# Kernel optimization log

Measured on AMD Instinct MI355X. Metric: run time of the kernel, lower is better.

Reference implementation:

```python
import jax, jax.numpy as jnp
import numpy as np


def _skew(w):
    # w: (..., 3) -> (..., 3, 3)
    wx, wy, wz = w[..., 0], w[..., 1], w[..., 2]
    z = jnp.zeros_like(wx)
    return jnp.stack([
        jnp.stack([z, -wz, wy], axis=-1),
        jnp.stack([wz, z, -wx], axis=-1),
        jnp.stack([-wy, wx, z], axis=-1),
    ], axis=-2)


def exp_se3(xi):
    # xi: (..., 6) se(3) coordinates [w, v] -> (..., 4, 4) SE(3) matrix exponential
    w = xi[..., :3]
    v = xi[..., 3:]
    th2 = jnp.sum(w * w, axis=-1)
    small = th2 < 1e-12
    th2_safe = jnp.where(small, 1.0, th2)
    th = jnp.sqrt(th2_safe)
    # Rodrigues coefficients with small-angle Taylor fallbacks
    A = jnp.where(small, 1.0 - th2 / 6.0, jnp.sin(th) / th)
    B = jnp.where(small, 0.5 - th2 / 24.0, (1.0 - jnp.cos(th)) / th2_safe)
    C = jnp.where(small, 1.0 / 6.0 - th2 / 120.0, (th - jnp.sin(th)) / (th2_safe * th))
    W = _skew(w)
    W2 = W @ W
    I3 = jnp.eye(3, dtype=xi.dtype)
    R = I3 + A[..., None, None] * W + B[..., None, None] * W2
    V = I3 + B[..., None, None] * W + C[..., None, None] * W2
    p = jnp.einsum('...ij,...j->...i', V, v)
    top = jnp.concatenate([R, p[..., None]], axis=-1)            # (..., 3, 4)
    bottom_row = jnp.array([0.0, 0.0, 0.0, 1.0], dtype=xi.dtype)
    bot = jnp.broadcast_to(bottom_row, top.shape[:-2] + (1, 4))  # (..., 1, 4)
    return jnp.concatenate([top, bot], axis=-2)


def setup_inputs() -> dict:
    key = jax.random.key(0)
    k1, k2, k3 = jax.random.split(key, 3)
    nBatch, nJoint = 262144, 24
    x = jax.random.normal(k1, (nBatch, nJoint), dtype=jnp.float32)
    # eta ~ U(-1, 1) per torch init (stdv = 1)
    eta = jax.random.uniform(k2, (nJoint, 6), dtype=jnp.float32, minval=-1.0, maxval=1.0)
    # M_se3 ~ U(-2, 2)
    M_se3 = jax.random.uniform(k3, (1, 6), dtype=jnp.float32, minval=-2.0, maxval=2.0)
    return {"x": x, "eta": eta, "M_se3": M_se3}


def reference(x, eta, M_se3):
    # x: (B, nJoint) joint angles; eta: (nJoint, 6) joint twists (useAdjoint=False);
    # M_se3: (1, 6) home pose in se(3).
    nBatch = x.shape[0]
    joint_twist = eta  # getJointTwist() with useAdjoint=False

    def step(T, inp):
        twist, ang = inp                                  # (6,), (B,)
        E = exp_se3(ang[:, None] * twist[None, :])        # (B, 4, 4)
        return T @ E, None

    T0 = jnp.broadcast_to(jnp.eye(4, dtype=x.dtype), (nBatch, 4, 4))
    T, _ = jax.lax.scan(step, T0, (joint_twist, x.T))
    return T @ exp_se3(M_se3)  # (B,4,4) @ (1,4,4) broadcasts over batch
```

## Files before the change

### kernel.cpp

```cpp
#include <hip/hip_runtime.h>

#define NJ   24
#define BLK  256
#define JREC 5
#define QMF4 (NJ * JREC)
#define NCPY (NJ * JREC + 2)
#define INV4PI 0.07957747154594767f

struct DQ { float w, x, y, z, t0, t1, t2; };

__device__ __forceinline__ DQ dq_comp(const DQ A, const DQ B) {
    const float u10 = A.y*B.t2 - A.z*B.t1;
    const float u11 = A.z*B.t0 - A.x*B.t2;
    const float u12 = A.x*B.t1 - A.y*B.t0;
    const float u20 = A.y*u12 - A.z*u11;
    const float u21 = A.z*u10 - A.x*u12;
    const float u22 = A.x*u11 - A.y*u10;
    const float tw  = 2.0f * A.w;
    DQ C;
    C.t0 = fmaf(tw, u10, fmaf(2.0f, u20, A.t0 + B.t0));
    C.t1 = fmaf(tw, u11, fmaf(2.0f, u21, A.t1 + B.t1));
    C.t2 = fmaf(tw, u12, fmaf(2.0f, u22, A.t2 + B.t2));
    C.w = A.w*B.w - A.x*B.x - A.y*B.y - A.z*B.z;
    C.x = A.w*B.x + A.x*B.w + A.y*B.z - A.z*B.y;
    C.y = A.w*B.y - A.x*B.z + A.y*B.w + A.z*B.x;
    C.z = A.w*B.z + A.x*B.y - A.y*B.x + A.z*B.w;
    return C;
}

__device__ __forceinline__ DQ dq_exp(const float4 A4, const float4 B4,
                                     const float4 C4, const float4 D4,
                                     const float a) {
    const float hrev = a * B4.w;
    const float sh   = __builtin_amdgcn_sinf(hrev);
    const float ch   = __builtin_amdgcn_cosf(hrev);
    const float s    = 2.0f * sh * ch;
    const float cB   = 2.0f * sh * sh;
    const float phi  = a * A4.w;
    const float g    = phi - s;
    DQ e;
    e.w  = ch;
    e.x  = sh * A4.x;
    e.y  = sh * A4.y;
    e.z  = sh * A4.z;
    e.t0 = fmaf(a, B4.x, fmaf(cB, C4.x, g * D4.x));
    e.t1 = fmaf(a, B4.y, fmaf(cB, C4.y, g * D4.y));
    e.t2 = fmaf(a, B4.z, fmaf(cB, C4.z, g * D4.z));
    return e;
}

__global__ __launch_bounds__(BLK, 4)
void poe_main(const float* __restrict__ x,
              const float* __restrict__ eta,
              const float* __restrict__ M,
              float* __restrict__ out,
              int nBatch)
{
    __shared__ float4 sC[NCPY];
    float* sF = (float*)sC;

    const int t = threadIdx.x;
    if (t < NJ) {
        const float w0 = eta[t*6+0], w1 = eta[t*6+1], w2 = eta[t*6+2];
        const float v0 = eta[t*6+3], v1 = eta[t*6+4], v2 = eta[t*6+5];
        const float k  = w0*w0 + w1*w1 + w2*w2;
        const bool  sm = (k < 1e-12f);
        const float invsqk = sm ? 0.0f : rsqrtf(k);
        const float sqk    = k * invsqk;
        const float invk   = invsqk * invsqk;
        const float invk15 = invk * invsqk;
        const float c10 = w1*v2 - w2*v1;
        const float c11 = w2*v0 - w0*v2;
        const float c12 = w0*v1 - w1*v0;
        const float c20 = w1*c12 - w2*c11;
        const float c21 = w2*c10 - w0*c12;
        const float c22 = w0*c11 - w1*c10;
        float* r = sF + t * JREC * 4;
        r[0]  = w0*invsqk;  r[1]  = w1*invsqk;  r[2]  = w2*invsqk;  r[3]  = sqk;
        r[4]  = v0;         r[5]  = v1;         r[6]  = v2;         r[7]  = sqk * INV4PI;
        r[8]  = c10*invk;   r[9]  = c11*invk;   r[10] = c12*invk;   r[11] = 0.0f;
        r[12] = c20*invk15; r[13] = c21*invk15; r[14] = c22*invk15; r[15] = 0.0f;
    } else if (t == NJ) {
        const float w0 = M[0], w1 = M[1], w2 = M[2];
        const float v0 = M[3], v1 = M[4], v2 = M[5];
        const float t2 = w0*w0 + w1*w1 + w2*w2;
        const bool  sm = (t2 < 1e-12f);
        const float t2s  = sm ? 1.0f : t2;
        const float invt = rsqrtf(t2s);
        const float th   = t2s * invt;
        float s, c;
        __sincosf(th, &s, &c);
        const float invt2 = invt * invt;
        const float B = sm ? 0.5f        : (1.0f - c) * invt2;
        const float C = sm ? (1.0f/6.0f) : (th - s) * invt2 * invt;
        float sh, chh;
        __sincosf(0.5f * th, &sh, &chh);
        const float axs = sm ? 0.5f : sh * invt;
        float* r = sF + QMF4 * 4;
        r[0] = sm ? 1.0f : chh;
        r[1] = axs * w0;
        r[2] = axs * w1;
        r[3] = axs * w2;
        const float c10 = w1*v2 - w2*v1, c11 = w2*v0 - w0*v2, c12 = w0*v1 - w1*v0;
        const float c20 = w1*c12 - w2*c11, c21 = w2*c10 - w0*c12, c22 = w0*c11 - w1*c10;
        r[4] = v0 + B*c10 + C*c20;
        r[5] = v1 + B*c11 + C*c21;
        r[6] = v2 + B*c12 + C*c22;
        r[7] = 0.0f;
    }

    const int gid = blockIdx.x * BLK + t;
    const int row = gid >> 2;
    const int q   = gid & 3;
    const bool active = row < nBatch;

    float2 xa = make_float2(0.f,0.f), xb = xa, xc = xa;
    if (active) {
        const float2* xp = (const float2*)(x + (size_t)row * NJ + q * 6);
        xa = xp[0]; xb = xp[1]; xc = xp[2];
    }

    __syncthreads();

    const int cbase = q * 6 * JREC;

#define REC(JJ, S) sC[cbase + (JJ)*JREC + (S)]

    const DQ e0 = dq_exp(REC(0,0), REC(0,1), REC(0,2), REC(0,3), xa.x);
    const DQ e1 = dq_exp(REC(1,0), REC(1,1), REC(1,2), REC(1,3), xa.y);
    const DQ e2 = dq_exp(REC(2,0), REC(2,1), REC(2,2), REC(2,3), xb.x);
    const DQ e3 = dq_exp(REC(3,0), REC(3,1), REC(3,2), REC(3,3), xb.y);
    const DQ e4 = dq_exp(REC(4,0), REC(4,1), REC(4,2), REC(4,3), xc.x);
    const DQ e5 = dq_exp(REC(5,0), REC(5,1), REC(5,2), REC(5,3), xc.y);
#undef REC

    const DQ c01 = dq_comp(e0, e1);
    const DQ c23 = dq_comp(e2, e3);
    const DQ c45 = dq_comp(e4, e5);
    const DQ c03 = dq_comp(c01, c23);
    DQ T = dq_comp(c03, c45);

#define COMBINE(BIT) do {                                                     \
    DQ O;                                                                     \
    O.w  = __shfl_xor(T.w,  BIT);  O.x  = __shfl_xor(T.x,  BIT);              \
    O.y  = __shfl_xor(T.y,  BIT);  O.z  = __shfl_xor(T.z,  BIT);              \
    O.t0 = __shfl_xor(T.t0, BIT);  O.t1 = __shfl_xor(T.t1, BIT);              \
    O.t2 = __shfl_xor(T.t2, BIT);                                             \
    const bool up = (q & (BIT)) != 0;          \
    DQ A, B;                                                                  \
    A.w  = up ? O.w  : T.w;   B.w  = up ? T.w  : O.w;                         \
    A.x  = up ? O.x  : T.x;   B.x  = up ? T.x  : O.x;                         \
    A.y  = up ? O.y  : T.y;   B.y  = up ? T.y  : O.y;                         \
    A.z  = up ? O.z  : T.z;   B.z  = up ? T.z  : O.z;                         \
    A.t0 = up ? O.t0 : T.t0;  B.t0 = up ? T.t0 : O.t0;                        \
    A.t1 = up ? O.t1 : T.t1;  B.t1 = up ? T.t1 : O.t1;                        \
    A.t2 = up ? O.t2 : T.t2;  B.t2 = up ? T.t2 : O.t2;                        \
    T = dq_comp(A, B);                                                        \
} while (0)

    COMBINE(1);
    COMBINE(2);
#undef COMBINE

    {
        const float4 Qm = sC[QMF4];
        const float4 Pm = sC[QMF4 + 1];
        DQ Em;
        Em.w = Qm.x; Em.x = Qm.y; Em.y = Qm.z; Em.z = Qm.w;
        Em.t0 = Pm.x; Em.t1 = Pm.y; Em.t2 = Pm.z;
        T = dq_comp(T, Em);
    }

    if (active) {
        const float xx = T.x*T.x, yy = T.y*T.y, zz = T.z*T.z;
        const float xy = T.x*T.y, xz = T.x*T.z, yz = T.y*T.z;
        const float wx = T.w*T.x, wy = T.w*T.y, wz = T.w*T.z;
        const float R00 = 1.0f - 2.0f*(yy + zz);
        const float R01 = 2.0f*(xy - wz);
        const float R02 = 2.0f*(xz + wy);
        const float R10 = 2.0f*(xy + wz);
        const float R11 = 1.0f - 2.0f*(xx + zz);
        const float R12 = 2.0f*(yz - wx);
        const float R20 = 2.0f*(xz - wy);
        const float R21 = 2.0f*(yz + wx);
        const float R22 = 1.0f - 2.0f*(xx + yy);

        float4 mine;
        if      (q == 0) mine = make_float4(R00, R01, R02, T.t0);
        else if (q == 1) mine = make_float4(R10, R11, R12, T.t1);
        else if (q == 2) mine = make_float4(R20, R21, R22, T.t2);
        else             mine = make_float4(0.0f, 0.0f, 0.0f, 1.0f);

        ((float4*)out)[(size_t)row * 4 + q] = mine;
    }
}

extern "C" void kernel_launch(void* const* d_in, const int* in_sizes, int n_in,
                              void* d_out, int out_size, void* d_ws, size_t ws_size,
                              hipStream_t stream)
{
    const float* x   = (const float*)d_in[0];
    const float* eta = (const float*)d_in[1];
    const float* M   = (const float*)d_in[2];
    float* out = (float*)d_out;

    const int nBatch   = in_sizes[0] / NJ;
    const int nThreads = nBatch * 4;
    const int grid     = (nThreads + BLK - 1) / BLK;

    poe_main<<<grid, BLK, 0, stream>>>(x, eta, M, out, nBatch);
}
```

Measured before the change: 21.24 us.

## Process four rows per thread with register-cached joint constants and prefetch

```diff
diff --git a/kernel.cpp b/kernel.cpp
--- a/kernel.cpp
+++ b/kernel.cpp
@@ -2,12 +2,16 @@
 
 #define NJ   24
 #define BLK  256
+#define W    4
 #define JREC 5
 #define QMF4 (NJ * JREC)
 #define NCPY (NJ * JREC + 2)
 #define INV4PI 0.07957747154594767f
+#define FOURPI 12.566370614359172f
 
 struct DQ { float w, x, y, z, t0, t1, t2; };
+
+struct JC { float W0,W1,W2,h, v0,v1,v2, c10,c11,c12, c20,c21,c22; };
 
 __device__ __forceinline__ DQ dq_comp(const DQ A, const DQ B) {
     const float u10 = A.y*B.t2 - A.z*B.t1;
@@ -28,24 +32,21 @@
     return C;
 }
 
-__device__ __forceinline__ DQ dq_exp(const float4 A4, const float4 B4,
-                                     const float4 C4, const float4 D4,
-                                     const float a) {
-    const float hrev = a * B4.w;
+__device__ __forceinline__ DQ dq_exp(const JC J, const float a) {
+    const float hrev = a * J.h;
     const float sh   = __builtin_amdgcn_sinf(hrev);
     const float ch   = __builtin_amdgcn_cosf(hrev);
     const float s    = 2.0f * sh * ch;
     const float cB   = 2.0f * sh * sh;
-    const float phi  = a * A4.w;
-    const float g    = phi - s;
+    const float g    = fmaf(FOURPI, hrev, -s);
     DQ e;
     e.w  = ch;
-    e.x  = sh * A4.x;
-    e.y  = sh * A4.y;
-    e.z  = sh * A4.z;
-    e.t0 = fmaf(a, B4.x, fmaf(cB, C4.x, g * D4.x));
-    e.t1 = fmaf(a, B4.y, fmaf(cB, C4.y, g * D4.y));
-    e.t2 = fmaf(a, B4.z, fmaf(cB, C4.z, g * D4.z));
+    e.x  = sh * J.W0;
+    e.y  = sh * J.W1;
+    e.z  = sh * J.W2;
+    e.t0 = fmaf(a, J.v0, fmaf(cB, J.c10, g * J.c20));
+    e.t1 = fmaf(a, J.v1, fmaf(cB, J.c11, g * J.c21));
+    e.t2 = fmaf(a, J.v2, fmaf(cB, J.c12, g * J.c22));
     return e;
 }
 
@@ -109,89 +110,105 @@
         r[7] = 0.0f;
     }
 
-    const int gid = blockIdx.x * BLK + t;
-    const int row = gid >> 2;
-    const int q   = gid & 3;
-    const bool active = row < nBatch;
-
+    const int gid    = blockIdx.x * BLK + t;
+    const int tq     = gid >> 2;
+    const int q      = gid & 3;
+    const int stride = (gridDim.x * BLK) >> 2;
+
+    __syncthreads();
+
+    JC jc[6];
+    const int cbase = q * 6 * JREC;
+    #pragma unroll
+    for (int j = 0; j < 6; ++j) {
+        const float4 A4 = sC[cbase + j*JREC + 0];
+        const float4 B4 = sC[cbase + j*JREC + 1];
+        const float4 C4 = sC[cbase + j*JREC + 2];
+        const float4 D4 = sC[cbase + j*JREC + 3];
+        jc[j].W0 = A4.x; jc[j].W1 = A4.y; jc[j].W2 = A4.z; jc[j].h = B4.w;
+        jc[j].v0 = B4.x; jc[j].v1 = B4.y; jc[j].v2 = B4.z;
+        jc[j].c10 = C4.x; jc[j].c11 = C4.y; jc[j].c12 = C4.z;
+        jc[j].c20 = D4.x; jc[j].c21 = D4.y; jc[j].c22 = D4.z;
+    }
+
+    const float4 Qm = sC[QMF4];
+    const float4 Pm = sC[QMF4 + 1];
+    DQ Em;
+    Em.w = Qm.x; Em.x = Qm.y; Em.y = Qm.z; Em.z = Qm.w;
+    Em.t0 = Pm.x; Em.t1 = Pm.y; Em.t2 = Pm.z;
+
+    int row = tq;
     float2 xa = make_float2(0.f,0.f), xb = xa, xc = xa;
-    if (active) {
+    if (row < nBatch) {
         const float2* xp = (const float2*)(x + (size_t)row * NJ + q * 6);
         xa = xp[0]; xb = xp[1]; xc = xp[2];
     }
 
-    __syncthreads();
-
-    const int cbase = q * 6 * JREC;
-
-#define REC(JJ, S) sC[cbase + (JJ)*JREC + (S)]
-
-    const DQ e0 = dq_exp(REC(0,0), REC(0,1), REC(0,2), REC(0,3), xa.x);
-    const DQ e1 = dq_exp(REC(1,0), REC(1,1), REC(1,2), REC(1,3), xa.y);
-    const DQ e2 = dq_exp(REC(2,0), REC(2,1), REC(2,2), REC(2,3), xb.x);
-    const DQ e3 = dq_exp(REC(3,0), REC(3,1), REC(3,2), REC(3,3), xb.y);
-    const DQ e4 = dq_exp(REC(4,0), REC(4,1), REC(4,2), REC(4,3), xc.x);
-    const DQ e5 = dq_exp(REC(5,0), REC(5,1), REC(5,2), REC(5,3), xc.y);
-#undef REC
-
-    const DQ c01 = dq_comp(e0, e1);
-    const DQ c23 = dq_comp(e2, e3);
-    const DQ c45 = dq_comp(e4, e5);
-    const DQ c03 = dq_comp(c01, c23);
-    DQ T = dq_comp(c03, c45);
+    #pragma unroll
+    for (int i = 0; i < W; ++i) {
+        const int nrow = row + stride;
+        float2 nxa = make_float2(0.f,0.f), nxb = nxa, nxc = nxa;
+        if (i < W-1 && nrow < nBatch) {
+            const float2* xp = (const float2*)(x + (size_t)nrow * NJ + q * 6);
+            nxa = xp[0]; nxb = xp[1]; nxc = xp[2];
+        }
+
+        DQ T = dq_exp(jc[0], xa.x);
+        T = dq_comp(T, dq_exp(jc[1], xa.y));
+        T = dq_comp(T, dq_exp(jc[2], xb.x));
+        T = dq_comp(T, dq_exp(jc[3], xb.y));
+        T = dq_comp(T, dq_exp(jc[4], xc.x));
+        T = dq_comp(T, dq_exp(jc[5], xc.y));
 
 #define COMBINE(BIT) do {                                                     \
-    DQ O;                                                                     \
-    O.w  = __shfl_xor(T.w,  BIT);  O.x  = __shfl_xor(T.x,  BIT);              \
-    O.y  = __shfl_xor(T.y,  BIT);  O.z  = __shfl_xor(T.z,  BIT);              \
-    O.t0 = __shfl_xor(T.t0, BIT);  O.t1 = __shfl_xor(T.t1, BIT);              \
-    O.t2 = __shfl_xor(T.t2, BIT);                                             \
-    const bool up = (q & (BIT)) != 0;          \
-    DQ A, B;                                                                  \
-    A.w  = up ? O.w  : T.w;   B.w  = up ? T.w  : O.w;                         \
-    A.x  = up ? O.x  : T.x;   B.x  = up ? T.x  : O.x;                         \
-    A.y  = up ? O.y  : T.y;   B.y  = up ? T.y  : O.y;                         \
-    A.z  = up ? O.z  : T.z;   B.z  = up ? T.z  : O.z;                         \
-    A.t0 = up ? O.t0 : T.t0;  B.t0 = up ? T.t0 : O.t0;                        \
-    A.t1 = up ? O.t1 : T.t1;  B.t1 = up ? T.t1 : O.t1;                        \
-    A.t2 = up ? O.t2 : T.t2;  B.t2 = up ? T.t2 : O.t2;                        \
-    T = dq_comp(A, B);                                                        \
+        DQ O;                                                                 \
+        O.w  = __shfl_xor(T.w,  BIT);  O.x  = __shfl_xor(T.x,  BIT);          \
+        O.y  = __shfl_xor(T.y,  BIT);  O.z  = __shfl_xor(T.z,  BIT);          \
+        O.t0 = __shfl_xor(T.t0, BIT);  O.t1 = __shfl_xor(T.t1, BIT);          \
+        O.t2 = __shfl_xor(T.t2, BIT);                                         \
+        const bool up = (q & (BIT)) != 0;      \
+        DQ A, B;                                                              \
+        A.w  = up ? O.w  : T.w;   B.w  = up ? T.w  : O.w;                     \
+        A.x  = up ? O.x  : T.x;   B.x  = up ? T.x  : O.x;                     \
+        A.y  = up ? O.y  : T.y;   B.y  = up ? T.y  : O.y;                     \
+        A.z  = up ? O.z  : T.z;   B.z  = up ? T.z  : O.z;                     \
+        A.t0 = up ? O.t0 : T.t0;  B.t0 = up ? T.t0 : O.t0;                    \
+        A.t1 = up ? O.t1 : T.t1;  B.t1 = up ? T.t1 : O.t1;                    \
+        A.t2 = up ? O.t2 : T.t2;  B.t2 = up ? T.t2 : O.t2;                    \
+        T = dq_comp(A, B);                                                    \
 } while (0)
 
-    COMBINE(1);
-    COMBINE(2);
+        COMBINE(1);
+        COMBINE(2);
 #undef COMBINE
 
-    {
-        const float4 Qm = sC[QMF4];
-        const float4 Pm = sC[QMF4 + 1];
-        DQ Em;
-        Em.w = Qm.x; Em.x = Qm.y; Em.y = Qm.z; Em.z = Qm.w;
-        Em.t0 = Pm.x; Em.t1 = Pm.y; Em.t2 = Pm.z;
         T = dq_comp(T, Em);
-    }
-
-    if (active) {
-        const float xx = T.x*T.x, yy = T.y*T.y, zz = T.z*T.z;
-        const float xy = T.x*T.y, xz = T.x*T.z, yz = T.y*T.z;
-        const float wx = T.w*T.x, wy = T.w*T.y, wz = T.w*T.z;
-        const float R00 = 1.0f - 2.0f*(yy + zz);
-        const float R01 = 2.0f*(xy - wz);
-        const float R02 = 2.0f*(xz + wy);
-        const float R10 = 2.0f*(xy + wz);
-        const float R11 = 1.0f - 2.0f*(xx + zz);
-        const float R12 = 2.0f*(yz - wx);
-        const float R20 = 2.0f*(xz - wy);
-        const float R21 = 2.0f*(yz + wx);
-        const float R22 = 1.0f - 2.0f*(xx + yy);
-
-        float4 mine;
-        if      (q == 0) mine = make_float4(R00, R01, R02, T.t0);
-        else if (q == 1) mine = make_float4(R10, R11, R12, T.t1);
-        else if (q == 2) mine = make_float4(R20, R21, R22, T.t2);
-        else             mine = make_float4(0.0f, 0.0f, 0.0f, 1.0f);
-
-        ((float4*)out)[(size_t)row * 4 + q] = mine;
+
+        if (row < nBatch) {
+            const float xx = T.x*T.x, yy = T.y*T.y, zz = T.z*T.z;
+            const float xy = T.x*T.y, xz = T.x*T.z, yz = T.y*T.z;
+            const float wx = T.w*T.x, wy = T.w*T.y, wz = T.w*T.z;
+            const float R00 = 1.0f - 2.0f*(yy + zz);
+            const float R01 = 2.0f*(xy - wz);
+            const float R02 = 2.0f*(xz + wy);
+            const float R10 = 2.0f*(xy + wz);
+            const float R11 = 1.0f - 2.0f*(xx + zz);
+            const float R12 = 2.0f*(yz - wx);
+            const float R20 = 2.0f*(xz - wy);
+            const float R21 = 2.0f*(yz + wx);
+            const float R22 = 1.0f - 2.0f*(xx + yy);
+
+            float4 mine;
+            if      (q == 0) mine = make_float4(R00, R01, R02, T.t0);
+            else if (q == 1) mine = make_float4(R10, R11, R12, T.t1);
+            else if (q == 2) mine = make_float4(R20, R21, R22, T.t2);
+            else             mine = make_float4(0.0f, 0.0f, 0.0f, 1.0f);
+
+            ((float4*)out)[(size_t)row * 4 + q] = mine;
+        }
+
+        row = nrow;
+        xa = nxa; xb = nxb; xc = nxc;
     }
 }
 
@@ -205,7 +222,8 @@
     float* out = (float*)d_out;
 
     const int nBatch   = in_sizes[0] / NJ;
-    const int nThreads = nBatch * 4;
+    const int nQuads   = (nBatch + W - 1) / W;
+    const int nThreads = nQuads * 4;
     const int grid     = (nThreads + BLK - 1) / BLK;
 
     poe_main<<<grid, BLK, 0, stream>>>(x, eta, M, out, nBatch);
```

Measured after the change: 24.59 us. 1.16x slower.

## Assign joint groups per wavefront, broadcast twist constants via readlane, reduce through LDS

Applied to the files above, without the earlier changes.

```diff
diff --git a/kernel.cpp b/kernel.cpp
--- a/kernel.cpp
+++ b/kernel.cpp
@@ -2,12 +2,16 @@
 
 #define NJ   24
 #define BLK  256
-#define JREC 5
-#define QMF4 (NJ * JREC)
-#define NCPY (NJ * JREC + 2)
+#define RPB  64
+#define SDS  36
 #define INV4PI 0.07957747154594767f
+#define FOURPI 12.566370614359172f
 
 struct DQ { float w, x, y, z, t0, t1, t2; };
+
+__device__ __forceinline__ float rdl(float v, int l) {
+    return __int_as_float(__builtin_amdgcn_readlane(__float_as_int(v), l));
+}
 
 __device__ __forceinline__ DQ dq_comp(const DQ A, const DQ B) {
     const float u10 = A.y*B.t2 - A.z*B.t1;
@@ -28,62 +32,99 @@
     return C;
 }
 
-__device__ __forceinline__ DQ dq_exp(const float4 A4, const float4 B4,
-                                     const float4 C4, const float4 D4,
-                                     const float a) {
-    const float hrev = a * B4.w;
+__device__ __forceinline__ DQ dq_exp(float W0, float W1, float W2, float hh,
+                                     float v0, float v1, float v2,
+                                     float c10, float c11, float c12,
+                                     float c20, float c21, float c22,
+                                     float a) {
+    const float hrev = a * hh;
     const float sh   = __builtin_amdgcn_sinf(hrev);
     const float ch   = __builtin_amdgcn_cosf(hrev);
     const float s    = 2.0f * sh * ch;
     const float cB   = 2.0f * sh * sh;
-    const float phi  = a * A4.w;
-    const float g    = phi - s;
+    const float g    = fmaf(FOURPI, hrev, -s);
     DQ e;
     e.w  = ch;
-    e.x  = sh * A4.x;
-    e.y  = sh * A4.y;
-    e.z  = sh * A4.z;
-    e.t0 = fmaf(a, B4.x, fmaf(cB, C4.x, g * D4.x));
-    e.t1 = fmaf(a, B4.y, fmaf(cB, C4.y, g * D4.y));
-    e.t2 = fmaf(a, B4.z, fmaf(cB, C4.z, g * D4.z));
+    e.x  = sh * W0;
+    e.y  = sh * W1;
+    e.z  = sh * W2;
+    e.t0 = fmaf(a, v0, fmaf(cB, c10, g * c20));
+    e.t1 = fmaf(a, v1, fmaf(cB, c11, g * c21));
+    e.t2 = fmaf(a, v2, fmaf(cB, c12, g * c22));
     return e;
 }
 
-__global__ __launch_bounds__(BLK, 4)
+__global__ __launch_bounds__(BLK, 8)
 void poe_main(const float* __restrict__ x,
               const float* __restrict__ eta,
               const float* __restrict__ M,
               float* __restrict__ out,
               int nBatch)
 {
-    __shared__ float4 sC[NCPY];
-    float* sF = (float*)sC;
+    __shared__ float sD[RPB * SDS];
 
-    const int t = threadIdx.x;
-    if (t < NJ) {
-        const float w0 = eta[t*6+0], w1 = eta[t*6+1], w2 = eta[t*6+2];
-        const float v0 = eta[t*6+3], v1 = eta[t*6+4], v2 = eta[t*6+5];
-        const float k  = w0*w0 + w1*w1 + w2*w2;
+    const int t    = threadIdx.x;
+    const int lane = t & 63;
+    const int w    = __builtin_amdgcn_readfirstlane(t >> 6);
+
+    const int row  = blockIdx.x * RPB + lane;
+    const bool active = row < nBatch;
+
+    float2 xa = make_float2(0.f,0.f), xb = xa, xc = xa;
+    if (active) {
+        const float2* xp = (const float2*)(x + (size_t)row * NJ + w * 6);
+        xa = xp[0]; xb = xp[1]; xc = xp[2];
+    }
+
+    float W0,W1,W2,hh, v0,v1,v2, c10,c11,c12, c20,c21,c22;
+    {
+        const int jj = w*6 + (lane < 6 ? lane : 0);
+        const float e0 = eta[jj*6+0], e1 = eta[jj*6+1], e2 = eta[jj*6+2];
+        const float e3 = eta[jj*6+3], e4 = eta[jj*6+4], e5 = eta[jj*6+5];
+        const float k  = e0*e0 + e1*e1 + e2*e2;
         const bool  sm = (k < 1e-12f);
         const float invsqk = sm ? 0.0f : rsqrtf(k);
         const float sqk    = k * invsqk;
         const float invk   = invsqk * invsqk;
         const float invk15 = invk * invsqk;
-        const float c10 = w1*v2 - w2*v1;
-        const float c11 = w2*v0 - w0*v2;
-        const float c12 = w0*v1 - w1*v0;
-        const float c20 = w1*c12 - w2*c11;
-        const float c21 = w2*c10 - w0*c12;
-        const float c22 = w0*c11 - w1*c10;
-        float* r = sF + t * JREC * 4;
-        r[0]  = w0*invsqk;  r[1]  = w1*invsqk;  r[2]  = w2*invsqk;  r[3]  = sqk;
-        r[4]  = v0;         r[5]  = v1;         r[6]  = v2;         r[7]  = sqk * INV4PI;
-        r[8]  = c10*invk;   r[9]  = c11*invk;   r[10] = c12*invk;   r[11] = 0.0f;
-        r[12] = c20*invk15; r[13] = c21*invk15; r[14] = c22*invk15; r[15] = 0.0f;
-    } else if (t == NJ) {
-        const float w0 = M[0], w1 = M[1], w2 = M[2];
-        const float v0 = M[3], v1 = M[4], v2 = M[5];
-        const float t2 = w0*w0 + w1*w1 + w2*w2;
+        W0 = e0*invsqk; W1 = e1*invsqk; W2 = e2*invsqk;
+        hh = sqk * INV4PI;
+        v0 = e3; v1 = e4; v2 = e5;
+        const float a0 = e1*e5 - e2*e4;
+        const float a1 = e2*e3 - e0*e5;
+        const float a2 = e0*e4 - e1*e3;
+        c10 = a0*invk;  c11 = a1*invk;  c12 = a2*invk;
+        c20 = (e1*a2 - e2*a1)*invk15;
+        c21 = (e2*a0 - e0*a2)*invk15;
+        c22 = (e0*a1 - e1*a0)*invk15;
+    }
+
+#define EXPJ(J, A_) dq_exp(rdl(W0,J), rdl(W1,J), rdl(W2,J), rdl(hh,J),       \
+                           rdl(v0,J), rdl(v1,J), rdl(v2,J),                  \
+                           rdl(c10,J), rdl(c11,J), rdl(c12,J),               \
+                           rdl(c20,J), rdl(c21,J), rdl(c22,J), (A_))
+
+    DQ T = EXPJ(0, xa.x);
+    T = dq_comp(T, EXPJ(1, xa.y));
+    T = dq_comp(T, EXPJ(2, xb.x));
+    T = dq_comp(T, EXPJ(3, xb.y));
+    T = dq_comp(T, EXPJ(4, xc.x));
+    T = dq_comp(T, EXPJ(5, xc.y));
+#undef EXPJ
+
+    {
+        float4* dst = (float4*)(sD + lane*SDS + w*8);
+        dst[0] = make_float4(T.w, T.x, T.y, T.z);
+        dst[1] = make_float4(T.t0, T.t1, T.t2, 0.0f);
+    }
+    __syncthreads();
+
+    if (w != 0) return;
+
+    DQ Em;
+    {
+        const float m0=M[0], m1=M[1], m2=M[2], m3=M[3], m4=M[4], m5=M[5];
+        const float t2 = m0*m0 + m1*m1 + m2*m2;
         const bool  sm = (t2 < 1e-12f);
         const float t2s  = sm ? 1.0f : t2;
         const float invt = rsqrtf(t2s);
@@ -96,102 +137,40 @@
         float sh, chh;
         __sincosf(0.5f * th, &sh, &chh);
         const float axs = sm ? 0.5f : sh * invt;
-        float* r = sF + QMF4 * 4;
-        r[0] = sm ? 1.0f : chh;
-        r[1] = axs * w0;
-        r[2] = axs * w1;
-        r[3] = axs * w2;
-        const float c10 = w1*v2 - w2*v1, c11 = w2*v0 - w0*v2, c12 = w0*v1 - w1*v0;
-        const float c20 = w1*c12 - w2*c11, c21 = w2*c10 - w0*c12, c22 = w0*c11 - w1*c10;
-        r[4] = v0 + B*c10 + C*c20;
-        r[5] = v1 + B*c11 + C*c21;
-        r[6] = v2 + B*c12 + C*c22;
-        r[7] = 0.0f;
+        Em.w = sm ? 1.0f : chh;
+        Em.x = axs * m0;  Em.y = axs * m1;  Em.z = axs * m2;
+        const float a0 = m1*m5 - m2*m4, a1 = m2*m3 - m0*m5, a2 = m0*m4 - m1*m3;
+        const float b0 = m1*a2 - m2*a1, b1 = m2*a0 - m0*a2, b2 = m0*a1 - m1*a0;
+        Em.t0 = m3 + B*a0 + C*b0;
+        Em.t1 = m4 + B*a1 + C*b1;
+        Em.t2 = m5 + B*a2 + C*b2;
     }
 
-    const int gid = blockIdx.x * BLK + t;
-    const int row = gid >> 2;
-    const int q   = gid & 3;
-    const bool active = row < nBatch;
-
-    float2 xa = make_float2(0.f,0.f), xb = xa, xc = xa;
-    if (active) {
-        const float2* xp = (const float2*)(x + (size_t)row * NJ + q * 6);
-        xa = xp[0]; xb = xp[1]; xc = xp[2];
+    const float* src = sD + lane*SDS;
+    DQ D[4];
+    #pragma unroll
+    for (int k = 0; k < 4; ++k) {
+        const float4 qq = ((const float4*)(src + k*8))[0];
+        const float4 tt = ((const float4*)(src + k*8))[1];
+        D[k].w = qq.x; D[k].x = qq.y; D[k].y = qq.z; D[k].z = qq.w;
+        D[k].t0 = tt.x; D[k].t1 = tt.y; D[k].t2 = tt.z;
     }
 
-    __syncthreads();
-
-    const int cbase = q * 6 * JREC;
-
-#define REC(JJ, S) sC[cbase + (JJ)*JREC + (S)]
-
-    const DQ e0 = dq_exp(REC(0,0), REC(0,1), REC(0,2), REC(0,3), xa.x);
-    const DQ e1 = dq_exp(REC(1,0), REC(1,1), REC(1,2), REC(1,3), xa.y);
-    const DQ e2 = dq_exp(REC(2,0), REC(2,1), REC(2,2), REC(2,3), xb.x);
-    const DQ e3 = dq_exp(REC(3,0), REC(3,1), REC(3,2), REC(3,3), xb.y);
-    const DQ e4 = dq_exp(REC(4,0), REC(4,1), REC(4,2), REC(4,3), xc.x);
-    const DQ e5 = dq_exp(REC(5,0), REC(5,1), REC(5,2), REC(5,3), xc.y);
-#undef REC
-
-    const DQ c01 = dq_comp(e0, e1);
-    const DQ c23 = dq_comp(e2, e3);
-    const DQ c45 = dq_comp(e4, e5);
-    const DQ c03 = dq_comp(c01, c23);
-    DQ T = dq_comp(c03, c45);
-
-#define COMBINE(BIT) do {                                                     \
-    DQ O;                                                                     \
-    O.w  = __shfl_xor(T.w,  BIT);  O.x  = __shfl_xor(T.x,  BIT);              \
-    O.y  = __shfl_xor(T.y,  BIT);  O.z  = __shfl_xor(T.z,  BIT);              \
-    O.t0 = __shfl_xor(T.t0, BIT);  O.t1 = __shfl_xor(T.t1, BIT);              \
-    O.t2 = __shfl_xor(T.t2, BIT);                                             \
-    const bool up = (q & (BIT)) != 0;          \
-    DQ A, B;                                                                  \
-    A.w  = up ? O.w  : T.w;   B.w  = up ? T.w  : O.w;                         \
-    A.x  = up ? O.x  : T.x;   B.x  = up ? T.x  : O.x;                         \
-    A.y  = up ? O.y  : T.y;   B.y  = up ? T.y  : O.y;                         \
-    A.z  = up ? O.z  : T.z;   B.z  = up ? T.z  : O.z;                         \
-    A.t0 = up ? O.t0 : T.t0;  B.t0 = up ? T.t0 : O.t0;                        \
-    A.t1 = up ? O.t1 : T.t1;  B.t1 = up ? T.t1 : O.t1;                        \
-    A.t2 = up ? O.t2 : T.t2;  B.t2 = up ? T.t2 : O.t2;                        \
-    T = dq_comp(A, B);                                                        \
-} while (0)
-
-    COMBINE(1);
-    COMBINE(2);
-#undef COMBINE
-
-    {
-        const float4 Qm = sC[QMF4];
-        const float4 Pm = sC[QMF4 + 1];
-        DQ Em;
-        Em.w = Qm.x; Em.x = Qm.y; Em.y = Qm.z; Em.z = Qm.w;
-        Em.t0 = Pm.x; Em.t1 = Pm.y; Em.t2 = Pm.z;
-        T = dq_comp(T, Em);
-    }
+    DQ F = dq_comp(dq_comp(D[0], D[1]), dq_comp(D[2], D[3]));
+    F = dq_comp(F, Em);
 
     if (active) {
-        const float xx = T.x*T.x, yy = T.y*T.y, zz = T.z*T.z;
-        const float xy = T.x*T.y, xz = T.x*T.z, yz = T.y*T.z;
-        const float wx = T.w*T.x, wy = T.w*T.y, wz = T.w*T.z;
-        const float R00 = 1.0f - 2.0f*(yy + zz);
-        const float R01 = 2.0f*(xy - wz);
-        const float R02 = 2.0f*(xz + wy);
-        const float R10 = 2.0f*(xy + wz);
-        const float R11 = 1.0f - 2.0f*(xx + zz);
-        const float R12 = 2.0f*(yz - wx);
-        const float R20 = 2.0f*(xz - wy);
-        const float R21 = 2.0f*(yz + wx);
-        const float R22 = 1.0f - 2.0f*(xx + yy);
-
-        float4 mine;
-        if      (q == 0) mine = make_float4(R00, R01, R02, T.t0);
-        else if (q == 1) mine = make_float4(R10, R11, R12, T.t1);
-        else if (q == 2) mine = make_float4(R20, R21, R22, T.t2);
-        else             mine = make_float4(0.0f, 0.0f, 0.0f, 1.0f);
-
-        ((float4*)out)[(size_t)row * 4 + q] = mine;
+        const float xx = F.x*F.x, yy = F.y*F.y, zz = F.z*F.z;
+        const float xy = F.x*F.y, xz = F.x*F.z, yz = F.y*F.z;
+        const float wx = F.w*F.x, wy = F.w*F.y, wz = F.w*F.z;
+        float4* o = (float4*)(out + (size_t)row * 16);
+        o[0] = make_float4(1.0f - 2.0f*(yy + zz), 2.0f*(xy - wz),
+                           2.0f*(xz + wy),        F.t0);
+        o[1] = make_float4(2.0f*(xy + wz),        1.0f - 2.0f*(xx + zz),
+                           2.0f*(yz - wx),        F.t1);
+        o[2] = make_float4(2.0f*(xz - wy),        2.0f*(yz + wx),
+                           1.0f - 2.0f*(xx + yy), F.t2);
+        o[3] = make_float4(0.0f, 0.0f, 0.0f, 1.0f);
     }
 }
 
@@ -204,9 +183,8 @@
     const float* M   = (const float*)d_in[2];
     float* out = (float*)d_out;
 
-    const int nBatch   = in_sizes[0] / NJ;
-    const int nThreads = nBatch * 4;
-    const int grid     = (nThreads + BLK - 1) / BLK;
+    const int nBatch = in_sizes[0] / NJ;
+    const int grid   = (nBatch + RPB - 1) / RPB;
 
     poe_main<<<grid, BLK, 0, stream>>>(x, eta, M, out, nBatch);
 }
```

After: 24.81 us. 16.8% more time.

## Process two batch rows per thread quad and shrink per-joint shared record

Applied to the files above, without the earlier changes.

```diff
diff --git a/kernel.cpp b/kernel.cpp
--- a/kernel.cpp
+++ b/kernel.cpp
@@ -2,10 +2,10 @@
 
 #define NJ   24
 #define BLK  256
-#define JREC 5
-#define QMF4 (NJ * JREC)
-#define NCPY (NJ * JREC + 2)
+#define QMF4 (NJ * 3)
+#define NCPY (NJ * 3 + 2)
 #define INV4PI 0.07957747154594767f
+#define FOURPI 12.566370614359172f
 
 struct DQ { float w, x, y, z, t0, t1, t2; };
 
@@ -29,24 +29,58 @@
 }
 
 __device__ __forceinline__ DQ dq_exp(const float4 A4, const float4 B4,
-                                     const float4 C4, const float4 D4,
-                                     const float a) {
-    const float hrev = a * B4.w;
+                                     const float4 C4,
+                                     float c20, float c21, float c22,
+                                     float a) {
+    const float hrev = a * A4.w;
     const float sh   = __builtin_amdgcn_sinf(hrev);
     const float ch   = __builtin_amdgcn_cosf(hrev);
     const float s    = 2.0f * sh * ch;
     const float cB   = 2.0f * sh * sh;
-    const float phi  = a * A4.w;
-    const float g    = phi - s;
+    const float g    = fmaf(FOURPI, hrev, -s);
     DQ e;
     e.w  = ch;
     e.x  = sh * A4.x;
     e.y  = sh * A4.y;
     e.z  = sh * A4.z;
-    e.t0 = fmaf(a, B4.x, fmaf(cB, C4.x, g * D4.x));
-    e.t1 = fmaf(a, B4.y, fmaf(cB, C4.y, g * D4.y));
-    e.t2 = fmaf(a, B4.z, fmaf(cB, C4.z, g * D4.z));
+    e.t0 = fmaf(a, B4.x, fmaf(cB, C4.x, g * c20));
+    e.t1 = fmaf(a, B4.y, fmaf(cB, C4.y, g * c21));
+    e.t2 = fmaf(a, B4.z, fmaf(cB, C4.z, g * c22));
     return e;
+}
+
+__device__ __forceinline__ DQ quad_combine(DQ T, const int q) {
+    #pragma unroll
+    for (int bit = 1; bit <= 2; bit <<= 1) {
+        DQ O;
+        O.w  = __shfl_xor(T.w,  bit);  O.x  = __shfl_xor(T.x,  bit);
+        O.y  = __shfl_xor(T.y,  bit);  O.z  = __shfl_xor(T.z,  bit);
+        O.t0 = __shfl_xor(T.t0, bit);  O.t1 = __shfl_xor(T.t1, bit);
+        O.t2 = __shfl_xor(T.t2, bit);
+        const bool up = (q & bit) != 0;
+        DQ A, B;
+        A.w  = up ? O.w  : T.w;   B.w  = up ? T.w  : O.w;
+        A.x  = up ? O.x  : T.x;   B.x  = up ? T.x  : O.x;
+        A.y  = up ? O.y  : T.y;   B.y  = up ? T.y  : O.y;
+        A.z  = up ? O.z  : T.z;   B.z  = up ? T.z  : O.z;
+        A.t0 = up ? O.t0 : T.t0;  B.t0 = up ? T.t0 : O.t0;
+        A.t1 = up ? O.t1 : T.t1;  B.t1 = up ? T.t1 : O.t1;
+        A.t2 = up ? O.t2 : T.t2;  B.t2 = up ? T.t2 : O.t2;
+        T = dq_comp(A, B);
+    }
+    return T;
+}
+
+__device__ __forceinline__ float4 row_of(const DQ F, const int q) {
+    const float xx = F.x*F.x, yy = F.y*F.y, zz = F.z*F.z;
+    const float xy = F.x*F.y, xz = F.x*F.z, yz = F.y*F.z;
+    const float wx = F.w*F.x, wy = F.w*F.y, wz = F.w*F.z;
+    float4 r;
+    if      (q == 0) r = make_float4(1.0f-2.0f*(yy+zz), 2.0f*(xy-wz), 2.0f*(xz+wy), F.t0);
+    else if (q == 1) r = make_float4(2.0f*(xy+wz), 1.0f-2.0f*(xx+zz), 2.0f*(yz-wx), F.t1);
+    else if (q == 2) r = make_float4(2.0f*(xz-wy), 2.0f*(yz+wx), 1.0f-2.0f*(xx+yy), F.t2);
+    else             r = make_float4(0.0f, 0.0f, 0.0f, 1.0f);
+    return r;
 }
 
 __global__ __launch_bounds__(BLK, 4)
@@ -68,18 +102,14 @@
         const float invsqk = sm ? 0.0f : rsqrtf(k);
         const float sqk    = k * invsqk;
         const float invk   = invsqk * invsqk;
-        const float invk15 = invk * invsqk;
-        const float c10 = w1*v2 - w2*v1;
-        const float c11 = w2*v0 - w0*v2;
-        const float c12 = w0*v1 - w1*v0;
-        const float c20 = w1*c12 - w2*c11;
-        const float c21 = w2*c10 - w0*c12;
-        const float c22 = w0*c11 - w1*c10;
-        float* r = sF + t * JREC * 4;
-        r[0]  = w0*invsqk;  r[1]  = w1*invsqk;  r[2]  = w2*invsqk;  r[3]  = sqk;
-        r[4]  = v0;         r[5]  = v1;         r[6]  = v2;         r[7]  = sqk * INV4PI;
-        r[8]  = c10*invk;   r[9]  = c11*invk;   r[10] = c12*invk;   r[11] = 0.0f;
-        r[12] = c20*invk15; r[13] = c21*invk15; r[14] = c22*invk15; r[15] = 0.0f;
+        float* r = sF + t * 12;
+        r[0]  = w0*invsqk;        r[1]  = w1*invsqk;
+        r[2]  = w2*invsqk;        r[3]  = sqk * INV4PI;
+        r[4]  = v0;  r[5]  = v1;  r[6]  = v2;  r[7] = 0.0f;
+        r[8]  = (w1*v2 - w2*v1)*invk;
+        r[9]  = (w2*v0 - w0*v2)*invk;
+        r[10] = (w0*v1 - w1*v0)*invk;
+        r[11] = 0.0f;
     } else if (t == NJ) {
         const float w0 = M[0], w1 = M[1], w2 = M[2];
         const float v0 = M[3], v1 = M[4], v2 = M[5];
@@ -98,101 +128,75 @@
         const float axs = sm ? 0.5f : sh * invt;
         float* r = sF + QMF4 * 4;
         r[0] = sm ? 1.0f : chh;
-        r[1] = axs * w0;
-        r[2] = axs * w1;
-        r[3] = axs * w2;
-        const float c10 = w1*v2 - w2*v1, c11 = w2*v0 - w0*v2, c12 = w0*v1 - w1*v0;
-        const float c20 = w1*c12 - w2*c11, c21 = w2*c10 - w0*c12, c22 = w0*c11 - w1*c10;
-        r[4] = v0 + B*c10 + C*c20;
-        r[5] = v1 + B*c11 + C*c21;
-        r[6] = v2 + B*c12 + C*c22;
+        r[1] = axs * w0;  r[2] = axs * w1;  r[3] = axs * w2;
+        const float a0 = w1*v2 - w2*v1, a1 = w2*v0 - w0*v2, a2 = w0*v1 - w1*v0;
+        const float b0 = w1*a2 - w2*a1, b1 = w2*a0 - w0*a2, b2 = w0*a1 - w1*a0;
+        r[4] = v0 + B*a0 + C*b0;
+        r[5] = v1 + B*a1 + C*b1;
+        r[6] = v2 + B*a2 + C*b2;
         r[7] = 0.0f;
     }
 
-    const int gid = blockIdx.x * BLK + t;
-    const int row = gid >> 2;
-    const int q   = gid & 3;
-    const bool active = row < nBatch;
-
-    float2 xa = make_float2(0.f,0.f), xb = xa, xc = xa;
-    if (active) {
-        const float2* xp = (const float2*)(x + (size_t)row * NJ + q * 6);
-        xa = xp[0]; xb = xp[1]; xc = xp[2];
+    const int gid  = blockIdx.x * BLK + t;
+    const int quad = gid >> 2;
+    const int q    = gid & 3;
+    const int r0   = quad * 2;
+    const int r1   = r0 + 1;
+    const bool a0  = r0 < nBatch;
+    const bool a1  = r1 < nBatch;
+
+    float2 xa0 = make_float2(0.f,0.f), xb0 = xa0, xc0 = xa0;
+    float2 xa1 = xa0, xb1 = xa0, xc1 = xa0;
+    if (a0) {
+        const float2* xp = (const float2*)(x + (size_t)r0 * NJ + q * 6);
+        xa0 = xp[0]; xb0 = xp[1]; xc0 = xp[2];
+    }
+    if (a1) {
+        const float2* xp = (const float2*)(x + (size_t)r1 * NJ + q * 6);
+        xa1 = xp[0]; xb1 = xp[1]; xc1 = xp[2];
     }
 
     __syncthreads();
 
-    const int cbase = q * 6 * JREC;
-
-#define REC(JJ, S) sC[cbase + (JJ)*JREC + (S)]
-
-    const DQ e0 = dq_exp(REC(0,0), REC(0,1), REC(0,2), REC(0,3), xa.x);
-    const DQ e1 = dq_exp(REC(1,0), REC(1,1), REC(1,2), REC(1,3), xa.y);
-    const DQ e2 = dq_exp(REC(2,0), REC(2,1), REC(2,2), REC(2,3), xb.x);
-    const DQ e3 = dq_exp(REC(3,0), REC(3,1), REC(3,2), REC(3,3), xb.y);
-    const DQ e4 = dq_exp(REC(4,0), REC(4,1), REC(4,2), REC(4,3), xc.x);
-    const DQ e5 = dq_exp(REC(5,0), REC(5,1), REC(5,2), REC(5,3), xc.y);
-#undef REC
-
-    const DQ c01 = dq_comp(e0, e1);
-    const DQ c23 = dq_comp(e2, e3);
-    const DQ c45 = dq_comp(e4, e5);
-    const DQ c03 = dq_comp(c01, c23);
-    DQ T = dq_comp(c03, c45);
-
-#define COMBINE(BIT) do {                                                     \
-    DQ O;                                                                     \
-    O.w  = __shfl_xor(T.w,  BIT);  O.x  = __shfl_xor(T.x,  BIT);              \
-    O.y  = __shfl_xor(T.y,  BIT);  O.z  = __shfl_xor(T.z,  BIT);              \
-    O.t0 = __shfl_xor(T.t0, BIT);  O.t1 = __shfl_xor(T.t1, BIT);              \
-    O.t2 = __shfl_xor(T.t2, BIT);                                             \
-    const bool up = (q & (BIT)) != 0;          \
-    DQ A, B;                                                                  \
-    A.w  = up ? O.w  : T.w;   B.w  = up ? T.w  : O.w;                         \
-    A.x  = up ? O.x  : T.x;   B.x  = up ? T.x  : O.x;                         \
-    A.y  = up ? O.y  : T.y;   B.y  = up ? T.y  : O.y;                         \
-    A.z  = up ? O.z  : T.z;   B.z  = up ? T.z  : O.z;                         \
-    A.t0 = up ? O.t0 : T.t0;  B.t0 = up ? T.t0 : O.t0;                        \
-    A.t1 = up ? O.t1 : T.t1;  B.t1 = up ? T.t1 : O.t1;                        \
-    A.t2 = up ? O.t2 : T.t2;  B.t2 = up ? T.t2 : O.t2;                        \
-    T = dq_comp(A, B);                                                        \
+    const int cbase = q * 18;
+    DQ TA, TB;
+
+#define JSTEP(JJ, A0_, A1_, FIRST) do {                                       \
+    const float4 A4 = sC[cbase + (JJ)*3 + 0];                                 \
+    const float4 B4 = sC[cbase + (JJ)*3 + 1];                                 \
+    const float4 C4 = sC[cbase + (JJ)*3 + 2];                                 \
+    const float c20 = A4.y*C4.z - A4.z*C4.y;               \
+    const float c21 = A4.z*C4.x - A4.x*C4.z;                                  \
+    const float c22 = A4.x*C4.y - A4.y*C4.x;                                  \
+    const DQ eA = dq_exp(A4, B4, C4, c20, c21, c22, (A0_));                   \
+    const DQ eB = dq_exp(A4, B4, C4, c20, c21, c22, (A1_));                   \
+    if (FIRST) { TA = eA; TB = eB; }                                          \
+    else       { TA = dq_comp(TA, eA); TB = dq_comp(TB, eB); }                \
 } while (0)
 
-    COMBINE(1);
-    COMBINE(2);
-#undef COMBINE
-
+    JSTEP(0, xa0.x, xa1.x, true);
+    JSTEP(1, xa0.y, xa1.y, false);
+    JSTEP(2, xb0.x, xb1.x, false);
+    JSTEP(3, xb0.y, xb1.y, false);
+    JSTEP(4, xc0.x, xc1.x, false);
+    JSTEP(5, xc0.y, xc1.y, false);
+#undef JSTEP
+
+    TA = quad_combine(TA, q);
+    TB = quad_combine(TB, q);
+
+    DQ Em;
     {
         const float4 Qm = sC[QMF4];
         const float4 Pm = sC[QMF4 + 1];
-        DQ Em;
         Em.w = Qm.x; Em.x = Qm.y; Em.y = Qm.z; Em.z = Qm.w;
         Em.t0 = Pm.x; Em.t1 = Pm.y; Em.t2 = Pm.z;
-        T = dq_comp(T, Em);
-    }
-
-    if (active) {
-        const float xx = T.x*T.x, yy = T.y*T.y, zz = T.z*T.z;
-        const float xy = T.x*T.y, xz = T.x*T.z, yz = T.y*T.z;
-        const float wx = T.w*T.x, wy = T.w*T.y, wz = T.w*T.z;
-        const float R00 = 1.0f - 2.0f*(yy + zz);
-        const float R01 = 2.0f*(xy - wz);
-        const float R02 = 2.0f*(xz + wy);
-        const float R10 = 2.0f*(xy + wz);
-        const float R11 = 1.0f - 2.0f*(xx + zz);
-        const float R12 = 2.0f*(yz - wx);
-        const float R20 = 2.0f*(xz - wy);
-        const float R21 = 2.0f*(yz + wx);
-        const float R22 = 1.0f - 2.0f*(xx + yy);
-
-        float4 mine;
-        if      (q == 0) mine = make_float4(R00, R01, R02, T.t0);
-        else if (q == 1) mine = make_float4(R10, R11, R12, T.t1);
-        else if (q == 2) mine = make_float4(R20, R21, R22, T.t2);
-        else             mine = make_float4(0.0f, 0.0f, 0.0f, 1.0f);
-
-        ((float4*)out)[(size_t)row * 4 + q] = mine;
-    }
+    }
+    TA = dq_comp(TA, Em);
+    TB = dq_comp(TB, Em);
+
+    if (a0) ((float4*)out)[(size_t)r0 * 4 + q] = row_of(TA, q);
+    if (a1) ((float4*)out)[(size_t)r1 * 4 + q] = row_of(TB, q);
 }
 
 extern "C" void kernel_launch(void* const* d_in, const int* in_sizes, int n_in,
@@ -205,7 +209,8 @@
     float* out = (float*)d_out;
 
     const int nBatch   = in_sizes[0] / NJ;
-    const int nThreads = nBatch * 4;
+    const int nQuads   = (nBatch + 1) / 2;
+    const int nThreads = nQuads * 4;
     const int grid     = (nThreads + BLK - 1) / BLK;
 
     poe_main<<<grid, BLK, 0, stream>>>(x, eta, M, out, nBatch);
```

New measurement: 20.64 us. 2.8% less time.
